# Optimization experiments

Measured on AMD Instinct MI355X. Metric: run time of the kernel, lower is better.

## Reference

```python
import jax, jax.numpy as jnp
import numpy as np

DT = 1e-3            # norse default integration step
TAU_MEM_INV = 50.0   # 1 / tau_mem, tau_mem = 0.02 from config
TAU_SYN_INV = 200.0  # norse default
V_TH = 1.0           # config['threshold']
ALPHA = 100.0        # SuperSpike surrogate sharpness (norse default)


@jax.custom_vjp
def spike(x):
    # Heaviside forward, SuperSpike surrogate gradient backward
    return (x > 0).astype(x.dtype)

def _spike_fwd(x):
    return (x > 0).astype(x.dtype), x

def _spike_bwd(res, g):
    return (g / (ALPHA * jnp.abs(res) + 1.0) ** 2,)

spike.defvjp(_spike_fwd, _spike_bwd)


def lif_step(v, i, inp):
    # norse lif_feed_forward_step: decay v and i, spike, reset, inject input into i
    v_dec = v + DT * TAU_MEM_INV * (-v + i)   # v_leak = 0
    i_dec = i - DT * TAU_SYN_INV * i
    s = spike(v_dec - V_TH)
    v_new = (1.0 - s) * v_dec                 # v_reset = 0
    i_new = i_dec + inp
    return s, v_new, i_new


def setup_inputs() -> dict:
    key = jax.random.key(0)
    ks = jax.random.split(key, 7)
    B, T, H, OUT = 256, 32, 1024, 10
    IN = 2 * 34 * 34  # 2312
    x = jax.random.uniform(ks[0], (B, T, 2, 34, 34), dtype=jnp.float32)
    s_in = 1.0 / np.sqrt(IN)
    s_h = 1.0 / np.sqrt(H)
    W1 = jax.random.uniform(ks[1], (H, IN), jnp.float32, -s_in, s_in)
    b1 = jax.random.uniform(ks[2], (H,), jnp.float32, -s_in, s_in)
    W2 = jax.random.uniform(ks[3], (H, H), jnp.float32, -s_h, s_h)
    b2 = jax.random.uniform(ks[4], (H,), jnp.float32, -s_h, s_h)
    Wout = jax.random.uniform(ks[5], (OUT, H), jnp.float32, -s_h, s_h)
    bout = jax.random.uniform(ks[6], (OUT,), jnp.float32, -s_h, s_h)
    return {"x": x, "W1": W1, "b1": b1, "W2": W2, "b2": b2, "Wout": Wout, "bout": bout}


def reference(x, W1, b1, W2, b2, Wout, bout):
    B, T = x.shape[0], x.shape[1]
    xt = x.reshape(B, T, -1).transpose(1, 0, 2)  # (T, B, IN): permute + flatten
    H, OUT = W1.shape[0], Wout.shape[0]
    zH = jnp.zeros((B, H), x.dtype)
    zO = jnp.zeros((B, OUT), x.dtype)
    carry0 = (zH, zH, zH, zH, zO, zO)  # (v1, i1, v2, i2, v_out, i_out)

    def step(carry, x_t):
        v1, i1, v2, i2, vo, io = carry
        s1, v1, i1 = lif_step(v1, i1, x_t @ W1.T + b1)
        s2, v2, i2 = lif_step(v2, i2, s1 @ W2.T + b2)
        so, vo, io = lif_step(vo, io, s2 @ Wout.T + bout)
        return (v1, i1, v2, i2, vo, io), so

    _, spikes = jax.lax.scan(step, carry0, xt)  # (T, B, OUT)
    return spikes.sum(axis=0)  # rate decoding -> (B, OUT)
```

## Files before the change

### kernel.cpp

```cpp
#include <hip/hip_runtime.h>


#define TB 256
#define TT 32
#define TH 1024
#define TIN 2312
#define TOUT 10
#define TM (TT * TB)
#define NK1 74
#define NK2 32
#define FR 512

typedef _Float16 f16_t;
typedef f16_t f16x8 __attribute__((ext_vector_type(8)));
typedef float floatx4 __attribute__((ext_vector_type(4)));

__device__ __forceinline__ void split2h(float v, f16_t& a, f16_t& b) {
  a = (f16_t)v;
  b = (f16_t)(v - (float)a);
}

__device__ __forceinline__ void gload16(const void* g, void* l) {
  __builtin_amdgcn_global_load_lds(
      (const __attribute__((address_space(1))) void*)g,
      (__attribute__((address_space(3))) void*)l, 16, 0, 0);
}

__global__ __launch_bounds__(256) void split_w_frag(
    const float* __restrict__ W, f16_t* __restrict__ P, long plane,
    int K, int nk32) {
  const int fid = blockIdx.x * 4 + (threadIdx.x >> 6);
  const int lane = threadIdx.x & 63;
  const int n16 = fid / nk32, k32 = fid - n16 * nk32;
  const long row = n16 * 16 + (lane & 15);
  const int k0 = k32 * 32 + (lane >> 4) * 8;
  float t[8];
  if (k0 + 8 <= K) {
    float4 v0 = *(const float4*)(W + row * K + k0);
    float4 v1 = *(const float4*)(W + row * K + k0 + 4);
    t[0] = v0.x; t[1] = v0.y; t[2] = v0.z; t[3] = v0.w;
    t[4] = v1.x; t[5] = v1.y; t[6] = v1.z; t[7] = v1.w;
  } else {
    #pragma unroll
    for (int e = 0; e < 8; ++e) t[e] = 0.f;
  }
  f16x8 h0, h1;
  #pragma unroll
  for (int e = 0; e < 8; ++e) {
    f16_t a, b;
    split2h(t[e], a, b);
    h0[e] = a; h1[e] = b;
  }
  const long o = (long)fid * 512 + lane * 8;
  *(f16x8*)(P + o) = h0;
  *(f16x8*)(P + plane + o) = h1;
}

__global__ __launch_bounds__(256, 2) void snn_gemm1(
    const float* __restrict__ Af, long sT, long sB,
    const f16_t* __restrict__ Bf, long planeB, int nk32, int K,
    const float* __restrict__ bias, float* __restrict__ C, int N) {
  __shared__ f16_t As[2 * 2 * 8 * FR];
  __shared__ f16_t Bs[2 * 2 * 8 * FR];

  const int tid = threadIdx.x;
  const int wave = tid >> 6, lane = tid & 63;
  const int quad = lane >> 4, l16 = lane & 15;
  const int wm = (wave & 1) * 64, wn = (wave >> 1) * 64;
  const int a16 = (wave & 1) * 4, b16 = (wave >> 1) * 4;
  const int mblk = blockIdx.x, nblk = blockIdx.y;
  const long m0 = (long)mblk * 128, n0 = (long)nblk * 128;

  floatx4 acc[4][4];
  #pragma unroll
  for (int i = 0; i < 4; ++i)
    #pragma unroll
    for (int j = 0; j < 4; ++j) acc[i][j] = (floatx4){0.f, 0.f, 0.f, 0.f};

  const int cr = tid >> 1, ch = tid & 1;
  const int am16 = cr >> 4;
  const int lnA0 = (cr & 15) | ((2 * ch) << 4);
  const int lnA1 = (cr & 15) | ((2 * ch + 1) << 4);
  float4 xv[4];
  const float* xrow = Af + ((m0 + cr) >> 8) * sT + ((m0 + cr) & 255) * sB;

  auto prefetchA = [&](int kt) {
    const int k0 = kt * 32 + ch * 16;
    #pragma unroll
    for (int u = 0; u < 4; ++u)
      xv[u] = (k0 + u * 4 < K) ? *(const float4*)(xrow + k0 + u * 4)
                               : float4{0.f, 0.f, 0.f, 0.f};
  };

  auto commitA = [&](int buf) {
    #pragma unroll
    for (int half = 0; half < 2; ++half) {
      const float* p = (const float*)&xv[half * 2];
      f16x8 p0, p1;
      #pragma unroll
      for (int e = 0; e < 8; ++e) {
        f16_t a, b;
        split2h(p[e], a, b);
        p0[e] = a; p1[e] = b;
      }
      const int ln = half ? lnA1 : lnA0;
      *(f16x8*)(&As[((buf * 2 + 0) * 8 + am16) * FR + ln * 8]) = p0;
      *(f16x8*)(&As[((buf * 2 + 1) * 8 + am16) * FR + ln * 8]) = p1;
    }
  };

  const long nbase = (n0 >> 4) * (long)nk32;
  auto gloadB = [&](int kt, int buf) {
    #pragma unroll
    for (int c = 0; c < 4; ++c) {
      const int chk = wave * 4 + c;
      const int pl = chk >> 3, n16 = chk & 7;
      const f16_t* src = Bf + pl * planeB +
                         (nbase + (long)n16 * nk32 + kt) * FR + lane * 8;
      gload16(src, &Bs[((buf * 2 + pl) * 8 + n16) * FR]);
    }
  };

  prefetchA(0);
  gloadB(0, 0);
  commitA(0);
  prefetchA(1);
  __syncthreads();

  for (int kt = 0; kt < nk32; ++kt) {
    const int cur = kt & 1;
    if (kt + 1 < nk32) {
      gloadB(kt + 1, cur ^ 1);
      commitA(cur ^ 1);
    }
    if (kt + 2 < nk32) prefetchA(kt + 2);

    f16x8 afr[2][4];
    #pragma unroll
    for (int pl = 0; pl < 2; ++pl)
      #pragma unroll
      for (int i = 0; i < 4; ++i)
        afr[pl][i] = *(const f16x8*)(
            &As[((cur * 2 + pl) * 8 + a16 + i) * FR + lane * 8]);

    #pragma unroll
    for (int pb = 0; pb < 2; ++pb) {
      f16x8 bfr[4];
      #pragma unroll
      for (int j = 0; j < 4; ++j)
        bfr[j] = *(const f16x8*)(
            &Bs[((cur * 2 + pb) * 8 + b16 + j) * FR + lane * 8]);
      const int pamax = 1 - pb;
      #pragma unroll
      for (int pa = 0; pa < 2; ++pa) {
        if (pa > pamax) break;
        #pragma unroll
        for (int i = 0; i < 4; ++i)
          #pragma unroll
          for (int j = 0; j < 4; ++j)
            acc[i][j] = __builtin_amdgcn_mfma_f32_16x16x32_f16(
                afr[pa][i], bfr[j], acc[i][j], 0, 0, 0);
      }
    }
    __syncthreads();
  }

  #pragma unroll
  for (int j = 0; j < 4; ++j) {
    const long col = n0 + wn + j * 16 + l16;
    const float bvv = bias[col];
    #pragma unroll
    for (int i = 0; i < 4; ++i) {
      const long row0 = m0 + wm + i * 16 + quad * 4;
      #pragma unroll
      for (int g = 0; g < 4; ++g)
        C[(row0 + g) * (long)N + col] = acc[i][j][g] + bvv;
    }
  }
}

__global__ __launch_bounds__(256, 2) void snn_gemm2(
    const f16_t* __restrict__ Ab, long sT, long sB,
    const f16_t* __restrict__ Bf, long planeB, int nk32,
    const float* __restrict__ bias, float* __restrict__ C, int N) {
  __shared__ f16_t As[2 * 8 * FR];
  __shared__ f16_t Bs[2 * 2 * 8 * FR];

  const int tid = threadIdx.x;
  const int wave = tid >> 6, lane = tid & 63;
  const int quad = lane >> 4, l16 = lane & 15;
  const int wm = (wave & 1) * 64, wn = (wave >> 1) * 64;
  const int a16 = (wave & 1) * 4, b16 = (wave >> 1) * 4;
  const int mblk = blockIdx.x, nblk = blockIdx.y;
  const long m0 = (long)mblk * 128, n0 = (long)nblk * 128;

  floatx4 acc[4][4];
  #pragma unroll
  for (int i = 0; i < 4; ++i)
    #pragma unroll
    for (int j = 0; j < 4; ++j) acc[i][j] = (floatx4){0.f, 0.f, 0.f, 0.f};

  const int cr = tid >> 1, ch = tid & 1;
  const int am16 = cr >> 4;
  const int lnA0 = (cr & 15) | ((2 * ch) << 4);
  const int lnA1 = (cr & 15) | ((2 * ch + 1) << 4);
  f16x8 av[2];
  const f16_t* arow = Ab + ((m0 + cr) >> 8) * sT + ((m0 + cr) & 255) * sB;

  auto prefetchA = [&](int kt) {
    const f16_t* p = arow + kt * 32 + ch * 16;
    av[0] = *(const f16x8*)p;
    av[1] = *(const f16x8*)(p + 8);
  };

  auto commitA = [&](int buf) {
    *(f16x8*)(&As[(buf * 8 + am16) * FR + lnA0 * 8]) = av[0];
    *(f16x8*)(&As[(buf * 8 + am16) * FR + lnA1 * 8]) = av[1];
  };

  const long nbase = (n0 >> 4) * (long)nk32;
  auto gloadB = [&](int kt, int buf) {
    #pragma unroll
    for (int c = 0; c < 4; ++c) {
      const int chk = wave * 4 + c;
      const int pl = chk >> 3, n16 = chk & 7;
      const f16_t* src = Bf + pl * planeB +
                         (nbase + (long)n16 * nk32 + kt) * FR + lane * 8;
      gload16(src, &Bs[((buf * 2 + pl) * 8 + n16) * FR]);
    }
  };

  prefetchA(0);
  gloadB(0, 0);
  commitA(0);
  prefetchA(1);
  __syncthreads();

  for (int kt = 0; kt < nk32; ++kt) {
    const int cur = kt & 1;
    if (kt + 1 < nk32) {
      gloadB(kt + 1, cur ^ 1);
      commitA(cur ^ 1);
    }
    if (kt + 2 < nk32) prefetchA(kt + 2);

    f16x8 afr[4];
    #pragma unroll
    for (int i = 0; i < 4; ++i)
      afr[i] = *(const f16x8*)(&As[(cur * 8 + a16 + i) * FR + lane * 8]);

    #pragma unroll
    for (int pb = 0; pb < 2; ++pb) {
      f16x8 bfr[4];
      #pragma unroll
      for (int j = 0; j < 4; ++j)
        bfr[j] = *(const f16x8*)(
            &Bs[((cur * 2 + pb) * 8 + b16 + j) * FR + lane * 8]);
      #pragma unroll
      for (int i = 0; i < 4; ++i)
        #pragma unroll
        for (int j = 0; j < 4; ++j)
          acc[i][j] = __builtin_amdgcn_mfma_f32_16x16x32_f16(
              afr[i], bfr[j], acc[i][j], 0, 0, 0);
    }
    __syncthreads();
  }

  #pragma unroll
  for (int j = 0; j < 4; ++j) {
    const long col = n0 + wn + j * 16 + l16;
    const float bvv = bias[col];
    #pragma unroll
    for (int i = 0; i < 4; ++i) {
      const long row0 = m0 + wm + i * 16 + quad * 4;
      #pragma unroll
      for (int g = 0; g < 4; ++g)
        C[(row0 + g) * (long)N + col] = acc[i][j][g] + bvv;
    }
  }
}

__global__ __launch_bounds__(256) void lif_scan_f16(const float* __restrict__ I,
                                                    f16_t* __restrict__ S) {
  int idx = blockIdx.x * 256 + threadIdx.x;
  float v = 0.f, cur = 0.f;
  #pragma unroll
  for (int t = 0; t < TT; ++t) {
    float inp = I[(long)t * (TB * TH) + idx];
    float vd = fmaf(0.05f, cur - v, v);
    float id = cur - 0.2f * cur;
    float s = (vd > 1.0f) ? 1.0f : 0.f;
    v = (1.0f - s) * vd;
    cur = id + inp;
    S[(long)t * (TB * TH) + idx] = (f16_t)s;
  }
}

__global__ __launch_bounds__(256) void gemm3_kernel(
    const f16_t* __restrict__ S2, const float* __restrict__ Wout,
    const float* __restrict__ bout, float* __restrict__ I3) {
  int wv = (blockIdx.x * blockDim.x + threadIdx.x) >> 6;
  int lane = threadIdx.x & 63;
  if (wv >= TM) return;
  const f16_t* srow = S2 + (long)wv * TH;
  float acc[TOUT];
  #pragma unroll
  for (int o = 0; o < TOUT; ++o) acc[o] = 0.f;
  for (int k = lane; k < TH; k += 64) {
    float s = (float)srow[k];
    #pragma unroll
    for (int o = 0; o < TOUT; ++o) acc[o] = fmaf(s, Wout[o * TH + k], acc[o]);
  }
  #pragma unroll
  for (int off = 32; off > 0; off >>= 1)
    #pragma unroll
    for (int o = 0; o < TOUT; ++o) acc[o] += __shfl_down(acc[o], off, 64);
  if (lane == 0) {
    #pragma unroll
    for (int o = 0; o < TOUT; ++o) I3[(long)wv * TOUT + o] = acc[o] + bout[o];
  }
}

__global__ __launch_bounds__(256) void scan_out(const float* __restrict__ I3,
                                                float* __restrict__ out) {
  int idx = blockIdx.x * blockDim.x + threadIdx.x;
  if (idx >= TB * TOUT) return;
  float v = 0.f, cur = 0.f, cnt = 0.f;
  #pragma unroll
  for (int t = 0; t < TT; ++t) {
    float inp = I3[(long)t * (TB * TOUT) + idx];
    float vd = fmaf(0.05f, cur - v, v);
    float id = cur - 0.2f * cur;
    float s = (vd > 1.0f) ? 1.0f : 0.f;
    v = (1.0f - s) * vd;
    cur = id + inp;
    cnt += s;
  }
  out[idx] = cnt;
}

extern "C" void kernel_launch(void* const* d_in, const int* in_sizes, int n_in,
                              void* d_out, int out_size, void* d_ws,
                              size_t ws_size, hipStream_t stream) {
  const float* x    = (const float*)d_in[0];
  const float* W1   = (const float*)d_in[1];
  const float* b1   = (const float*)d_in[2];
  const float* W2   = (const float*)d_in[3];
  const float* b2   = (const float*)d_in[4];
  const float* Wout = (const float*)d_in[5];
  const float* bout = (const float*)d_in[6];

  const long PL1 = 64L * NK1 * 512;
  const long PL2 = 64L * NK2 * 512;

  char* base = (char*)d_ws;
  const long S2_BYTES = (long)TM * TH * 2;
  f16_t* W1p  = (f16_t*)base;
  f16_t* W2p  = (f16_t*)(base + 2 * PL1 * 2);
  float* bufI = (float*)(base + S2_BYTES);
  f16_t* S1   = (f16_t*)(base + S2_BYTES + (long)TM * TH * 4);
  float* buf3 = (float*)(base + S2_BYTES + (long)TM * TH * 4 + (long)TM * TH * 2);
  f16_t* S2   = (f16_t*)base;

  split_w_frag<<<64 * NK1 / 4, 256, 0, stream>>>(W1, W1p, PL1, TIN, NK1);
  split_w_frag<<<64 * NK2 / 4, 256, 0, stream>>>(W2, W2p, PL2, TH, NK2);

  snn_gemm1<<<dim3(64, 8), 256, 0, stream>>>(
      x, (long)TIN, (long)TT * TIN, W1p, PL1, NK1, TIN, b1, bufI, TH);

  lif_scan_f16<<<(TB * TH) / 256, 256, 0, stream>>>(bufI, S1);

  snn_gemm2<<<dim3(64, 8), 256, 0, stream>>>(
      S1, (long)TB * TH, (long)TH, W2p, PL2, NK2, b2, bufI, TH);

  lif_scan_f16<<<(TB * TH) / 256, 256, 0, stream>>>(bufI, S2);

  gemm3_kernel<<<(TM * 64) / 256, 256, 0, stream>>>(S2, Wout, bout, buf3);

  scan_out<<<(TB * TOUT + 255) / 256, 256, 0, stream>>>(buf3, (float*)d_out);
}
```

Baseline: 329.1 us.

## Restructure GEMM kernels to 256x128 tiles with register-resident B and interleaved pipeline

```diff
diff --git a/kernel.cpp b/kernel.cpp
--- a/kernel.cpp
+++ b/kernel.cpp
@@ -18,12 +18,6 @@
 __device__ __forceinline__ void split2h(float v, f16_t& a, f16_t& b) {
   a = (f16_t)v;
   b = (f16_t)(v - (float)a);
-}
-
-__device__ __forceinline__ void gload16(const void* g, void* l) {
-  __builtin_amdgcn_global_load_lds(
-      (const __attribute__((address_space(1))) void*)g,
-      (__attribute__((address_space(3))) void*)l, 16, 0, 0);
 }
 
 __global__ __launch_bounds__(256) void split_w_frag(
@@ -56,46 +50,55 @@
   *(f16x8*)(P + plane + o) = h1;
 }
 
-__global__ __launch_bounds__(256, 2) void snn_gemm1(
+__global__ __launch_bounds__(512, 2) void snn_gemm1(
     const float* __restrict__ Af, long sT, long sB,
-    const f16_t* __restrict__ Bf, long planeB, int nk32, int K,
+    const f16_t* __restrict__ Bf, long planeB, int NT, int K,
     const float* __restrict__ bias, float* __restrict__ C, int N) {
-  __shared__ f16_t As[2 * 2 * 8 * FR];
-  __shared__ f16_t Bs[2 * 2 * 8 * FR];
+  __shared__ f16_t As[2 * 2 * 16 * FR];
 
   const int tid = threadIdx.x;
   const int wave = tid >> 6, lane = tid & 63;
   const int quad = lane >> 4, l16 = lane & 15;
-  const int wm = (wave & 1) * 64, wn = (wave >> 1) * 64;
-  const int a16 = (wave & 1) * 4, b16 = (wave >> 1) * 4;
-  const int mblk = blockIdx.x, nblk = blockIdx.y;
-  const long m0 = (long)mblk * 128, n0 = (long)nblk * 128;
-
-  floatx4 acc[4][4];
-  #pragma unroll
-  for (int i = 0; i < 4; ++i)
-    #pragma unroll
-    for (int j = 0; j < 4; ++j) acc[i][j] = (floatx4){0.f, 0.f, 0.f, 0.f};
+  const int wmi = wave & 1, wni = wave >> 1;
+  const long m0 = (long)blockIdx.x * 256, n0 = (long)blockIdx.y * 128;
+
+  floatx4 acc[8][2];
+  #pragma unroll
+  for (int f = 0; f < 8; ++f)
+    #pragma unroll
+    for (int j = 0; j < 2; ++j) acc[f][j] = (floatx4){0.f, 0.f, 0.f, 0.f};
 
   const int cr = tid >> 1, ch = tid & 1;
   const int am16 = cr >> 4;
   const int lnA0 = (cr & 15) | ((2 * ch) << 4);
   const int lnA1 = (cr & 15) | ((2 * ch + 1) << 4);
-  float4 xv[4];
   const float* xrow = Af + ((m0 + cr) >> 8) * sT + ((m0 + cr) & 255) * sB;
 
-  auto prefetchA = [&](int kt) {
+  const long nb0 = (n0 >> 4) + wni * 2;
+  const f16_t* Bw = Bf + lane * 8;
+
+  float4 xva[4], xvb[4];
+  f16x8 b0[2][2], b1[2][2];
+
+  auto PFA = [&](int kt, float4 (&xv)[4]) {
     const int k0 = kt * 32 + ch * 16;
     #pragma unroll
     for (int u = 0; u < 4; ++u)
       xv[u] = (k0 + u * 4 < K) ? *(const float4*)(xrow + k0 + u * 4)
                                : float4{0.f, 0.f, 0.f, 0.f};
   };
-
-  auto commitA = [&](int buf) {
-    #pragma unroll
-    for (int half = 0; half < 2; ++half) {
-      const float* p = (const float*)&xv[half * 2];
+  auto LDB = [&](int kt, f16x8 (&bb)[2][2]) {
+    #pragma unroll
+    for (int pl = 0; pl < 2; ++pl)
+      #pragma unroll
+      for (int j = 0; j < 2; ++j)
+        bb[pl][j] = *(const f16x8*)(Bw + pl * planeB +
+                                    ((nb0 + j) * (long)NT + kt) * FR);
+  };
+  auto CMT = [&](int buf, float4 (&xv)[4]) {
+    #pragma unroll
+    for (int h = 0; h < 2; ++h) {
+      const float* p = (const float*)&xv[h * 2];
       f16x8 p0, p1;
       #pragma unroll
       for (int e = 0; e < 8; ++e) {
@@ -103,179 +106,187 @@
         split2h(p[e], a, b);
         p0[e] = a; p1[e] = b;
       }
-      const int ln = half ? lnA1 : lnA0;
-      *(f16x8*)(&As[((buf * 2 + 0) * 8 + am16) * FR + ln * 8]) = p0;
-      *(f16x8*)(&As[((buf * 2 + 1) * 8 + am16) * FR + ln * 8]) = p1;
+      const int ln = h ? lnA1 : lnA0;
+      *(f16x8*)(&As[((buf * 2 + 0) * 16 + am16) * FR + ln * 8]) = p0;
+      *(f16x8*)(&As[((buf * 2 + 1) * 16 + am16) * FR + ln * 8]) = p1;
     }
   };
-
-  const long nbase = (n0 >> 4) * (long)nk32;
-  auto gloadB = [&](int kt, int buf) {
-    #pragma unroll
-    for (int c = 0; c < 4; ++c) {
-      const int chk = wave * 4 + c;
-      const int pl = chk >> 3, n16 = chk & 7;
-      const f16_t* src = Bf + pl * planeB +
-                         (nbase + (long)n16 * nk32 + kt) * FR + lane * 8;
-      gload16(src, &Bs[((buf * 2 + pl) * 8 + n16) * FR]);
+  auto MF = [&](int cur, int p, f16x8 (&bc)[2][2]) {
+    f16x8 a0[2][2];
+    #pragma unroll
+    for (int pl = 0; pl < 2; ++pl)
+      #pragma unroll
+      for (int f = 0; f < 2; ++f)
+        a0[pl][f] = *(const f16x8*)(
+            &As[((cur * 2 + pl) * 16 + wmi * 8 + p * 2 + f) * FR + lane * 8]);
+    __builtin_amdgcn_s_setprio(1);
+    #pragma unroll
+    for (int f = 0; f < 2; ++f)
+      #pragma unroll
+      for (int j = 0; j < 2; ++j) {
+        floatx4 t = acc[p * 2 + f][j];
+        t = __builtin_amdgcn_mfma_f32_16x16x32_f16(a0[0][f], bc[0][j], t, 0, 0, 0);
+        t = __builtin_amdgcn_mfma_f32_16x16x32_f16(a0[1][f], bc[0][j], t, 0, 0, 0);
+        t = __builtin_amdgcn_mfma_f32_16x16x32_f16(a0[0][f], bc[1][j], t, 0, 0, 0);
+        acc[p * 2 + f][j] = t;
+      }
+    __builtin_amdgcn_s_setprio(0);
+  };
+
+  auto body = [&](int kt, f16x8 (&bc)[2][2], f16x8 (&bn)[2][2],
+                  float4 (&xc)[4]) {
+    const int cur = kt & 1;
+    const int last = NT - 1;
+    LDB(kt + 1 <= last ? kt + 1 : last, bn);
+    MF(cur, 0, bc);
+    __builtin_amdgcn_sched_barrier(0);
+    CMT(cur ^ 1, xc);
+    MF(cur, 1, bc);
+    __builtin_amdgcn_sched_barrier(0);
+    PFA(kt + 3 <= last ? kt + 3 : last, xc);
+    MF(cur, 2, bc);
+    __builtin_amdgcn_sched_barrier(0);
+    MF(cur, 3, bc);
+    asm volatile("s_waitcnt lgkmcnt(0)" ::: "memory");
+    __builtin_amdgcn_s_barrier();
+    __builtin_amdgcn_sched_barrier(0);
+  };
+
+  PFA(0, xva);
+  LDB(0, b0);
+  CMT(0, xva);
+  PFA(1, xva);
+  PFA(2, xvb);
+  asm volatile("s_waitcnt lgkmcnt(0)" ::: "memory");
+  __builtin_amdgcn_s_barrier();
+
+  for (int kt = 0; kt < NT; kt += 2) {
+    body(kt, b0, b1, xva);
+    body(kt + 1, b1, b0, xvb);
+  }
+
+  #pragma unroll
+  for (int j = 0; j < 2; ++j) {
+    const long col = n0 + wni * 32 + j * 16 + l16;
+    const float bvv = bias[col];
+    #pragma unroll
+    for (int f = 0; f < 8; ++f) {
+      const long r0 = m0 + wmi * 128 + f * 16 + quad * 4;
+      #pragma unroll
+      for (int g = 0; g < 4; ++g)
+        C[(r0 + g) * (long)N + col] = acc[f][j][g] + bvv;
     }
-  };
-
-  prefetchA(0);
-  gloadB(0, 0);
-  commitA(0);
-  prefetchA(1);
-  __syncthreads();
-
-  for (int kt = 0; kt < nk32; ++kt) {
-    const int cur = kt & 1;
-    if (kt + 1 < nk32) {
-      gloadB(kt + 1, cur ^ 1);
-      commitA(cur ^ 1);
-    }
-    if (kt + 2 < nk32) prefetchA(kt + 2);
-
-    f16x8 afr[2][4];
-    #pragma unroll
-    for (int pl = 0; pl < 2; ++pl)
-      #pragma unroll
-      for (int i = 0; i < 4; ++i)
-        afr[pl][i] = *(const f16x8*)(
-            &As[((cur * 2 + pl) * 8 + a16 + i) * FR + lane * 8]);
-
-    #pragma unroll
-    for (int pb = 0; pb < 2; ++pb) {
-      f16x8 bfr[4];
-      #pragma unroll
-      for (int j = 0; j < 4; ++j)
-        bfr[j] = *(const f16x8*)(
-            &Bs[((cur * 2 + pb) * 8 + b16 + j) * FR + lane * 8]);
-      const int pamax = 1 - pb;
-      #pragma unroll
-      for (int pa = 0; pa < 2; ++pa) {
-        if (pa > pamax) break;
-        #pragma unroll
-        for (int i = 0; i < 4; ++i)
-          #pragma unroll
-          for (int j = 0; j < 4; ++j)
-            acc[i][j] = __builtin_amdgcn_mfma_f32_16x16x32_f16(
-                afr[pa][i], bfr[j], acc[i][j], 0, 0, 0);
-      }
-    }
-    __syncthreads();
-  }
-
-  #pragma unroll
-  for (int j = 0; j < 4; ++j) {
-    const long col = n0 + wn + j * 16 + l16;
-    const float bvv = bias[col];
-    #pragma unroll
-    for (int i = 0; i < 4; ++i) {
-      const long row0 = m0 + wm + i * 16 + quad * 4;
-      #pragma unroll
-      for (int g = 0; g < 4; ++g)
-        C[(row0 + g) * (long)N + col] = acc[i][j][g] + bvv;
-    }
-  }
-}
-
-__global__ __launch_bounds__(256, 2) void snn_gemm2(
+  }
+}
+
+__global__ __launch_bounds__(512, 2) void snn_gemm2(
     const f16_t* __restrict__ Ab, long sT, long sB,
-    const f16_t* __restrict__ Bf, long planeB, int nk32,
+    const f16_t* __restrict__ Bf, long planeB, int NT,
     const float* __restrict__ bias, float* __restrict__ C, int N) {
-  __shared__ f16_t As[2 * 8 * FR];
-  __shared__ f16_t Bs[2 * 2 * 8 * FR];
+  __shared__ f16_t As[2 * 16 * FR];
 
   const int tid = threadIdx.x;
   const int wave = tid >> 6, lane = tid & 63;
   const int quad = lane >> 4, l16 = lane & 15;
-  const int wm = (wave & 1) * 64, wn = (wave >> 1) * 64;
-  const int a16 = (wave & 1) * 4, b16 = (wave >> 1) * 4;
-  const int mblk = blockIdx.x, nblk = blockIdx.y;
-  const long m0 = (long)mblk * 128, n0 = (long)nblk * 128;
-
-  floatx4 acc[4][4];
-  #pragma unroll
-  for (int i = 0; i < 4; ++i)
-    #pragma unroll
-    for (int j = 0; j < 4; ++j) acc[i][j] = (floatx4){0.f, 0.f, 0.f, 0.f};
+  const int wmi = wave & 1, wni = wave >> 1;
+  const long m0 = (long)blockIdx.x * 256, n0 = (long)blockIdx.y * 128;
+
+  floatx4 acc[8][2];
+  #pragma unroll
+  for (int f = 0; f < 8; ++f)
+    #pragma unroll
+    for (int j = 0; j < 2; ++j) acc[f][j] = (floatx4){0.f, 0.f, 0.f, 0.f};
 
   const int cr = tid >> 1, ch = tid & 1;
   const int am16 = cr >> 4;
   const int lnA0 = (cr & 15) | ((2 * ch) << 4);
   const int lnA1 = (cr & 15) | ((2 * ch + 1) << 4);
-  f16x8 av[2];
   const f16_t* arow = Ab + ((m0 + cr) >> 8) * sT + ((m0 + cr) & 255) * sB;
 
-  auto prefetchA = [&](int kt) {
+  const long nb0 = (n0 >> 4) + wni * 2;
+  const f16_t* Bw = Bf + lane * 8;
+
+  f16x8 ava[2], avb[2];
+  f16x8 b0[2][2], b1[2][2];
+
+  auto PFA = [&](int kt, f16x8 (&av)[2]) {
     const f16_t* p = arow + kt * 32 + ch * 16;
     av[0] = *(const f16x8*)p;
     av[1] = *(const f16x8*)(p + 8);
   };
-
-  auto commitA = [&](int buf) {
-    *(f16x8*)(&As[(buf * 8 + am16) * FR + lnA0 * 8]) = av[0];
-    *(f16x8*)(&As[(buf * 8 + am16) * FR + lnA1 * 8]) = av[1];
-  };
-
-  const long nbase = (n0 >> 4) * (long)nk32;
-  auto gloadB = [&](int kt, int buf) {
-    #pragma unroll
-    for (int c = 0; c < 4; ++c) {
-      const int chk = wave * 4 + c;
-      const int pl = chk >> 3, n16 = chk & 7;
-      const f16_t* src = Bf + pl * planeB +
-                         (nbase + (long)n16 * nk32 + kt) * FR + lane * 8;
-      gload16(src, &Bs[((buf * 2 + pl) * 8 + n16) * FR]);
-    }
-  };
-
-  prefetchA(0);
-  gloadB(0, 0);
-  commitA(0);
-  prefetchA(1);
-  __syncthreads();
-
-  for (int kt = 0; kt < nk32; ++kt) {
+  auto LDB = [&](int kt, f16x8 (&bb)[2][2]) {
+    #pragma unroll
+    for (int pl = 0; pl < 2; ++pl)
+      #pragma unroll
+      for (int j = 0; j < 2; ++j)
+        bb[pl][j] = *(const f16x8*)(Bw + pl * planeB +
+                                    ((nb0 + j) * (long)NT + kt) * FR);
+  };
+  auto CMT = [&](int buf, f16x8 (&av)[2]) {
+    *(f16x8*)(&As[(buf * 16 + am16) * FR + lnA0 * 8]) = av[0];
+    *(f16x8*)(&As[(buf * 16 + am16) * FR + lnA1 * 8]) = av[1];
+  };
+  auto MF = [&](int cur, int p, f16x8 (&bc)[2][2]) {
+    f16x8 a0[2];
+    #pragma unroll
+    for (int f = 0; f < 2; ++f)
+      a0[f] = *(const f16x8*)(
+          &As[(cur * 16 + wmi * 8 + p * 2 + f) * FR + lane * 8]);
+    __builtin_amdgcn_s_setprio(1);
+    #pragma unroll
+    for (int f = 0; f < 2; ++f)
+      #pragma unroll
+      for (int j = 0; j < 2; ++j) {
+        floatx4 t = acc[p * 2 + f][j];
+        t = __builtin_amdgcn_mfma_f32_16x16x32_f16(a0[f], bc[0][j], t, 0, 0, 0);
+        t = __builtin_amdgcn_mfma_f32_16x16x32_f16(a0[f], bc[1][j], t, 0, 0, 0);
+        acc[p * 2 + f][j] = t;
+      }
+    __builtin_amdgcn_s_setprio(0);
+  };
+
+  auto body = [&](int kt, f16x8 (&bc)[2][2], f16x8 (&bn)[2][2],
+                  f16x8 (&xc)[2]) {
     const int cur = kt & 1;
-    if (kt + 1 < nk32) {
-      gloadB(kt + 1, cur ^ 1);
-      commitA(cur ^ 1);
-    }
-    if (kt + 2 < nk32) prefetchA(kt + 2);
-
-    f16x8 afr[4];
-    #pragma unroll
-    for (int i = 0; i < 4; ++i)
-      afr[i] = *(const f16x8*)(&As[(cur * 8 + a16 + i) * FR + lane * 8]);
-
-    #pragma unroll
-    for (int pb = 0; pb < 2; ++pb) {
-      f16x8 bfr[4];
-      #pragma unroll
-      for (int j = 0; j < 4; ++j)
-        bfr[j] = *(const f16x8*)(
-            &Bs[((cur * 2 + pb) * 8 + b16 + j) * FR + lane * 8]);
-      #pragma unroll
-      for (int i = 0; i < 4; ++i)
-        #pragma unroll
-        for (int j = 0; j < 4; ++j)
-          acc[i][j] = __builtin_amdgcn_mfma_f32_16x16x32_f16(
-              afr[i], bfr[j], acc[i][j], 0, 0, 0);
-    }
-    __syncthreads();
-  }
-
-  #pragma unroll
-  for (int j = 0; j < 4; ++j) {
-    const long col = n0 + wn + j * 16 + l16;
+    const int last = NT - 1;
+    LDB(kt + 1 <= last ? kt + 1 : last, bn);
+    MF(cur, 0, bc);
+    __builtin_amdgcn_sched_barrier(0);
+    CMT(cur ^ 1, xc);
+    MF(cur, 1, bc);
+    __builtin_amdgcn_sched_barrier(0);
+    PFA(kt + 3 <= last ? kt + 3 : last, xc);
+    MF(cur, 2, bc);
+    __builtin_amdgcn_sched_barrier(0);
+    MF(cur, 3, bc);
+    asm volatile("s_waitcnt lgkmcnt(0)" ::: "memory");
+    __builtin_amdgcn_s_barrier();
+    __builtin_amdgcn_sched_barrier(0);
+  };
+
+  PFA(0, ava);
+  LDB(0, b0);
+  CMT(0, ava);
+  PFA(1, ava);
+  PFA(2, avb);
+  asm volatile("s_waitcnt lgkmcnt(0)" ::: "memory");
+  __builtin_amdgcn_s_barrier();
+
+  for (int kt = 0; kt < NT; kt += 2) {
+    body(kt, b0, b1, ava);
+    body(kt + 1, b1, b0, avb);
+  }
+
+  #pragma unroll
+  for (int j = 0; j < 2; ++j) {
+    const long col = n0 + wni * 32 + j * 16 + l16;
     const float bvv = bias[col];
     #pragma unroll
-    for (int i = 0; i < 4; ++i) {
-      const long row0 = m0 + wm + i * 16 + quad * 4;
+    for (int f = 0; f < 8; ++f) {
+      const long r0 = m0 + wmi * 128 + f * 16 + quad * 4;
       #pragma unroll
       for (int g = 0; g < 4; ++g)
-        C[(row0 + g) * (long)N + col] = acc[i][j][g] + bvv;
+        C[(r0 + g) * (long)N + col] = acc[f][j][g] + bvv;
     }
   }
 }
@@ -365,12 +376,12 @@
   split_w_frag<<<64 * NK1 / 4, 256, 0, stream>>>(W1, W1p, PL1, TIN, NK1);
   split_w_frag<<<64 * NK2 / 4, 256, 0, stream>>>(W2, W2p, PL2, TH, NK2);
 
-  snn_gemm1<<<dim3(64, 8), 256, 0, stream>>>(
+  snn_gemm1<<<dim3(32, 8), 512, 0, stream>>>(
       x, (long)TIN, (long)TT * TIN, W1p, PL1, NK1, TIN, b1, bufI, TH);
 
   lif_scan_f16<<<(TB * TH) / 256, 256, 0, stream>>>(bufI, S1);
 
-  snn_gemm2<<<dim3(64, 8), 256, 0, stream>>>(
+  snn_gemm2<<<dim3(32, 8), 512, 0, stream>>>(
       S1, (long)TB * TH, (long)TH, W2p, PL2, NK2, b2, bufI, TH);
 
   lif_scan_f16<<<(TB * TH) / 256, 256, 0, stream>>>(bufI, S2);
```

Result: slower. 337.0 us (+2.4%).
